# Optimization experiments

Hardware: AMD Instinct MI355X
Metric: run time of the kernel (lower is better)

## Reference

```python
import jax, jax.numpy as jnp
import numpy as np

X_DIM = 1024
HEADS = 16
EPS = 1e-5  # torch LayerNorm default


def setup_inputs() -> dict:
    key = jax.random.key(0)
    ks = jax.random.split(key, 4)
    B, N = 4, 1024
    x = jax.random.normal(ks[0], (B, N, X_DIM), jnp.float32)
    # torch nn.Linear weights are [out_features, in_features]; y = x @ W.T
    Wq = jax.random.normal(ks[1], (X_DIM, X_DIM), jnp.float32) * 0.02
    Wkv = jax.random.normal(ks[2], (2 * X_DIM, X_DIM), jnp.float32) * 0.02  # k_dim = x_dim + v_dim
    Wt = jax.random.normal(ks[3], (HEADS, HEADS), jnp.float32) * 0.25  # talk_h head-mixing
    ln_g = jnp.ones((HEADS,), jnp.float32)
    ln_b = jnp.zeros((HEADS,), jnp.float32)
    return {"x": x, "Wq": Wq, "Wkv": Wkv, "Wt": Wt, "ln_g": ln_g, "ln_b": ln_b}


def reference(x, Wq, Wkv, Wt, ln_g, ln_b):
    B, N, D = x.shape
    H = HEADS
    dh = D // H  # v head dim (= x head dim here since v_dim == x_dim)
    # projections
    q = (x @ Wq.T).reshape(B, N, H, dh).transpose(0, 2, 1, 3)  # b h i d
    kv = x @ Wkv.T  # [B, N, 2D]
    k = kv[..., :D].reshape(B, N, H, dh).transpose(0, 2, 1, 3)  # b h j d
    v = kv[..., D:].reshape(B, N, H, dh).transpose(0, 2, 1, 3)  # b h j d
    # scaled dot-product scores (scale uses x_dim, not head dim — faithful to source)
    dots = jnp.einsum('bhid,bhjd->bhij', q, k) * (D ** -0.5)
    w = jax.nn.softmax(dots, axis=-1)  # [B, H, N, N]
    # talk_h: ChSwap (transpose dims 1 and -1) -> Linear(heads) -> LayerNorm(heads) -> ChSwap
    wt = w.transpose(0, 3, 2, 1)  # b j i h
    wt = wt @ Wt.T
    mu = wt.mean(-1, keepdims=True)
    var = wt.var(-1, keepdims=True)
    wt = (wt - mu) / jnp.sqrt(var + EPS) * ln_g + ln_b
    w = wt.transpose(0, 3, 2, 1)  # back to b h i j
    # soft attention output
    attn = jnp.einsum('bhij,bhjd->bhid', w, v)
    # hard selection: argmax over keys, gather value rows
    idx = jnp.argmax(w, axis=-1)  # [B, H, N]
    hard = jnp.take_along_axis(v, jnp.broadcast_to(idx[..., None], idx.shape + (dh,)), axis=2)
    # straight-through: forward = hard, gradient flows through attn
    rtn = attn - jax.lax.stop_gradient(attn - hard)
    return rtn.transpose(0, 2, 1, 3).reshape(B, N, H * dh)
```

## Files before the change

### kernel.cpp

```cpp
#include <hip/hip_runtime.h>


#define FMA4(cc, av, bv) \
  cc.x = fmaf(av, bv.x, cc.x); cc.y = fmaf(av, bv.y, cc.y); \
  cc.z = fmaf(av, bv.z, cc.z); cc.w = fmaf(av, bv.w, cc.w);

__global__ __launch_bounds__(256) void qkv_gemm(
    const float* __restrict__ X, const float* __restrict__ Wq,
    const float* __restrict__ Wkv, float* __restrict__ qT,
    float* __restrict__ kT, float* __restrict__ V)
{
  __shared__ __align__(16) float As[16 * 132];
  __shared__ __align__(16) float Bs[16 * 132];
  __shared__ __align__(16) float tb[128 * 32];

  const int t  = threadIdx.x;
  const int bn = blockIdx.x;
  const int bm = blockIdx.y;
  const int m0 = bm * 128, n0 = bn * 128;
  const int ty = t >> 4, tx = t & 15;

  const float* Wbase = (n0 < 1024) ? Wq : Wkv;
  const int nw0 = (n0 < 1024) ? n0 : (n0 - 1024);

  float4 c2[8][2];
#pragma unroll
  for (int a = 0; a < 8; a++) {
    c2[a][0] = make_float4(0.f, 0.f, 0.f, 0.f);
    c2[a][1] = make_float4(0.f, 0.f, 0.f, 0.f);
  }

  const int lr = t >> 1;
  const int lh = t & 1;

  const float4* As4 = (const float4*)As;
  const float4* Bs4 = (const float4*)Bs;

  for (int kb = 0; kb < 64; kb++) {
    const int k0 = kb * 16;
    __syncthreads();
#pragma unroll
    for (int s = 0; s < 2; s++) {
      const int kk = lh * 8 + s * 4;
      float4 av = *(const float4*)&X[(size_t)(m0 + lr) * 1024 + k0 + kk];
      float4 bv = *(const float4*)&Wbase[(size_t)(nw0 + lr) * 1024 + k0 + kk];
      As[(kk + 0) * 132 + lr] = av.x;
      As[(kk + 1) * 132 + lr] = av.y;
      As[(kk + 2) * 132 + lr] = av.z;
      As[(kk + 3) * 132 + lr] = av.w;
      Bs[(kk + 0) * 132 + lr] = bv.x;
      Bs[(kk + 1) * 132 + lr] = bv.y;
      Bs[(kk + 2) * 132 + lr] = bv.z;
      Bs[(kk + 3) * 132 + lr] = bv.w;
    }
    __syncthreads();
#pragma unroll
    for (int kk = 0; kk < 16; kk++) {
      float4 a0 = As4[kk * 33 + ty * 2];
      float4 a1 = As4[kk * 33 + ty * 2 + 1];
      float4 b0 = Bs4[kk * 33 + tx];
      float4 b1 = Bs4[kk * 33 + 16 + tx];
      FMA4(c2[0][0], a0.x, b0); FMA4(c2[0][1], a0.x, b1);
      FMA4(c2[1][0], a0.y, b0); FMA4(c2[1][1], a0.y, b1);
      FMA4(c2[2][0], a0.z, b0); FMA4(c2[2][1], a0.z, b1);
      FMA4(c2[3][0], a0.w, b0); FMA4(c2[3][1], a0.w, b1);
      FMA4(c2[4][0], a1.x, b0); FMA4(c2[4][1], a1.x, b1);
      FMA4(c2[5][0], a1.y, b0); FMA4(c2[5][1], a1.y, b1);
      FMA4(c2[6][0], a1.z, b0); FMA4(c2[6][1], a1.z, b1);
      FMA4(c2[7][0], a1.w, b0); FMA4(c2[7][1], a1.w, b1);
    }
  }

  if (n0 >= 2048) {
    const int nv0 = n0 - 2048;
#pragma unroll
    for (int a = 0; a < 8; a++) {
      *(float4*)&V[(size_t)(m0 + ty * 8 + a) * 1024 + nv0 + tx * 4]      = c2[a][0];
      *(float4*)&V[(size_t)(m0 + ty * 8 + a) * 1024 + nv0 + 64 + tx * 4] = c2[a][1];
    }
    return;
  }

  float* T = (n0 < 1024) ? qT : kT;
  const int nt0 = (n0 < 1024) ? n0 : (n0 - 1024);
  const int bB = m0 >> 10;
  const int i0 = m0 & 1023;
#pragma unroll
  for (int r = 0; r < 4; r++) {
    __syncthreads();
    if ((tx >> 3) == (r & 1)) {
      const int c0 = (tx & 7) * 4;
#pragma unroll
      for (int a = 0; a < 8; a++) {
        const int m = ty * 8 + a;
        float4 val = c2[a][r >> 1];
        tb[m * 32 + ((c0 + 0 + m) & 31)] = val.x;
        tb[m * 32 + ((c0 + 1 + m) & 31)] = val.y;
        tb[m * 32 + ((c0 + 2 + m) & 31)] = val.z;
        tb[m * 32 + ((c0 + 3 + m) & 31)] = val.w;
      }
    }
    __syncthreads();
    const int nl = t >> 3, mq = t & 7;
    float* Trow = T + (size_t)(bB * 1024 + nt0 + (r >> 1) * 64 + (r & 1) * 32 + nl) * 1024 + i0;
#pragma unroll
    for (int l = 0; l < 4; l++) {
      const int mb = (l * 8 + mq) * 4;
      float4 o;
      o.x = tb[(mb + 0) * 32 + ((nl + mb + 0) & 31)];
      o.y = tb[(mb + 1) * 32 + ((nl + mb + 1) & 31)];
      o.z = tb[(mb + 2) * 32 + ((nl + mb + 2) & 31)];
      o.w = tb[(mb + 3) * 32 + ((nl + mb + 3) & 31)];
      *(float4*)(Trow + mb) = o;
    }
  }
}

__global__ __launch_bounds__(256) void attn_stats_v5(
    const float* __restrict__ qT, const float* __restrict__ kT,
    float* __restrict__ Mm, float* __restrict__ Ml)
{
  const int t  = threadIdx.x;
  const int bx = blockIdx.x;
  const int b  = bx >> 8;
  const int it = (bx >> 3) & 31;
  const int js = bx & 7;
  const int wv = t >> 6;
  const int l  = t & 63;
  const int ih = l >> 5;
  const int jg = l & 31;
  const int i0w = __builtin_amdgcn_readfirstlane(it * 32 + wv * 8);
  const int iq = i0w + ih * 4;
  const int jq = js * 128 + jg * 4;

  const float scale = 0.03125f;

  for (int h = 0; h < 16; h++) {
    const size_t base = (size_t)(b * 1024 + h * 64) * 1024;
    float4 acc[4];
#pragma unroll
    for (int ii = 0; ii < 4; ii++) acc[ii] = make_float4(0.f, 0.f, 0.f, 0.f);

#pragma unroll 4
    for (int d = 0; d < 64; d++) {
      const float4 qv = *(const float4*)(qT + base + (size_t)d * 1024 + iq);
      const float4 kv = *(const float4*)(kT + base + (size_t)d * 1024 + jq);
      FMA4(acc[0], qv.x, kv);
      FMA4(acc[1], qv.y, kv);
      FMA4(acc[2], qv.z, kv);
      FMA4(acc[3], qv.w, kv);
    }

#pragma unroll
    for (int ii = 0; ii < 4; ii++) {
      const float s0 = acc[ii].x * scale;
      const float s1 = acc[ii].y * scale;
      const float s2 = acc[ii].z * scale;
      const float s3 = acc[ii].w * scale;
      float mx = fmaxf(fmaxf(s0, s1), fmaxf(s2, s3));
      mx = fmaxf(mx, __shfl_xor(mx, 1));
      mx = fmaxf(mx, __shfl_xor(mx, 2));
      mx = fmaxf(mx, __shfl_xor(mx, 4));
      mx = fmaxf(mx, __shfl_xor(mx, 8));
      mx = fmaxf(mx, __shfl_xor(mx, 16));
      float ss = __expf(s0 - mx) + __expf(s1 - mx) +
                 __expf(s2 - mx) + __expf(s3 - mx);
      ss += __shfl_xor(ss, 1);
      ss += __shfl_xor(ss, 2);
      ss += __shfl_xor(ss, 4);
      ss += __shfl_xor(ss, 8);
      ss += __shfl_xor(ss, 16);
      if (jg == ii) {
        const int idx = (((b * 16 + h) * 1024 + iq + ii) << 3) + js;
        Mm[idx] = mx;
        Ml[idx] = ss;
      }
    }
  }
}

__global__ __launch_bounds__(256) void attn_stats_v6(
    const float* __restrict__ qT, const float* __restrict__ kT,
    float* __restrict__ Mm, float* __restrict__ Ml, float* __restrict__ Sp)
{
  const int t  = threadIdx.x;
  const int bx = blockIdx.x;
  const int b  = bx >> 8;
  const int it = (bx >> 3) & 31;
  const int js = bx & 7;
  const int wv = t >> 6;
  const int l  = t & 63;
  const int ih = l >> 5;
  const int jg = l & 31;
  const int i0w = __builtin_amdgcn_readfirstlane(it * 32 + wv * 8);
  const int iq = i0w + ih * 4;
  const int jq = js * 128 + jg * 4;

  const float scale = 0.03125f;

  for (int h = 0; h < 16; h++) {
    const size_t base = (size_t)(b * 1024 + h * 64) * 1024;
    float4 acc[4];
#pragma unroll
    for (int ii = 0; ii < 4; ii++) acc[ii] = make_float4(0.f, 0.f, 0.f, 0.f);

#pragma unroll 4
    for (int d = 0; d < 64; d++) {
      const float4 qv = *(const float4*)(qT + base + (size_t)d * 1024 + iq);
      const float4 kv = *(const float4*)(kT + base + (size_t)d * 1024 + jq);
      FMA4(acc[0], qv.x, kv);
      FMA4(acc[1], qv.y, kv);
      FMA4(acc[2], qv.z, kv);
      FMA4(acc[3], qv.w, kv);
    }

#pragma unroll
    for (int ii = 0; ii < 4; ii++) {
      const float s0 = acc[ii].x * scale;
      const float s1 = acc[ii].y * scale;
      const float s2 = acc[ii].z * scale;
      const float s3 = acc[ii].w * scale;
      float mx = fmaxf(fmaxf(s0, s1), fmaxf(s2, s3));
      mx = fmaxf(mx, __shfl_xor(mx, 1));
      mx = fmaxf(mx, __shfl_xor(mx, 2));
      mx = fmaxf(mx, __shfl_xor(mx, 4));
      mx = fmaxf(mx, __shfl_xor(mx, 8));
      mx = fmaxf(mx, __shfl_xor(mx, 16));
      const float e0 = __expf(s0 - mx);
      const float e1 = __expf(s1 - mx);
      const float e2 = __expf(s2 - mx);
      const float e3 = __expf(s3 - mx);
      *(float4*)&Sp[((size_t)((b * 16 + h) * 1024) + iq + ii) * 1024 + jq] =
          make_float4(e0, e1, e2, e3);
      float ss = e0 + e1 + e2 + e3;
      ss += __shfl_xor(ss, 1);
      ss += __shfl_xor(ss, 2);
      ss += __shfl_xor(ss, 4);
      ss += __shfl_xor(ss, 8);
      ss += __shfl_xor(ss, 16);
      if (jg == ii) {
        const int idx = (((b * 16 + h) * 1024 + iq + ii) << 3) + js;
        Mm[idx] = mx;
        Ml[idx] = ss;
      }
    }
  }
}

__device__ inline unsigned long long mkkey(float v, int j) {
  unsigned u = __float_as_uint(v);
  u = (u & 0x80000000u) ? ~u : (u | 0x80000000u);
  return ((unsigned long long)u << 32) | (unsigned)(1023 - j);
}

__global__ __launch_bounds__(256) void attn_select_v5(
    const float* __restrict__ qT, const float* __restrict__ kT,
    const float* __restrict__ Mm, const float* __restrict__ Ml,
    const float* __restrict__ Wt, const float* __restrict__ ln_g,
    const float* __restrict__ ln_b, unsigned long long* __restrict__ HiKey)
{
  __shared__ __align__(16) float smem[64 * 271 + 512];
  float* ptile = smem;
  float* mred  = smem + 64 * 271;
  float* rred  = mred + 256;

  const int t  = threadIdx.x;
  const int bx = blockIdx.x;
  const int b  = bx >> 10;
  const int it = (bx >> 4) & 63;
  const int js = bx & 15;
  const int i0 = it << 4;
  const int j0 = js << 6;

  const float scale = 0.03125f;

  {
    const int base = (((b * 16 + (t >> 4)) * 1024 + i0 + (t & 15)) << 3);
    const float4 ma = *(const float4*)&Mm[base];
    const float4 mb = *(const float4*)&Mm[base + 4];
    const float4 la = *(const float4*)&Ml[base];
    const float4 lb = *(const float4*)&Ml[base + 4];
    float M = fmaxf(fmaxf(fmaxf(ma.x, ma.y), fmaxf(ma.z, ma.w)),
                    fmaxf(fmaxf(mb.x, mb.y), fmaxf(mb.z, mb.w)));
    float L = la.x * __expf(ma.x - M) + la.y * __expf(ma.y - M) +
              la.z * __expf(ma.z - M) + la.w * __expf(ma.w - M) +
              lb.x * __expf(mb.x - M) + lb.y * __expf(mb.y - M) +
              lb.z * __expf(mb.z - M) + lb.w * __expf(mb.w - M);
    mred[t] = M;
    rred[t] = 1.0f / L;
  }
  __syncthreads();

  const int wv = t >> 6;
  const int l  = t & 63;
  const int jq = l & 15;
  const int ig = l >> 4;
  const int iq = i0 + ig * 4;
  const int jcol = j0 + jq * 4;

#pragma unroll
  for (int hl = 0; hl < 4; hl++) {
    const int h = wv * 4 + hl;
    const size_t base = (size_t)(b * 1024 + h * 64) * 1024;
    float4 acc[4];
#pragma unroll
    for (int ii = 0; ii < 4; ii++) acc[ii] = make_float4(0.f, 0.f, 0.f, 0.f);

#pragma unroll 4
    for (int d = 0; d < 64; d++) {
      const float4 qv = *(const float4*)(qT + base + (size_t)d * 1024 + iq);
      const float4 kv = *(const float4*)(kT + base + (size_t)d * 1024 + jcol);
      FMA4(acc[0], qv.x, kv);
      FMA4(acc[1], qv.y, kv);
      FMA4(acc[2], qv.z, kv);
      FMA4(acc[3], qv.w, kv);
    }

    const int hrot = (h + jq) & 15;
#pragma unroll
    for (int ii = 0; ii < 4; ii++) {
      const int iL = ig * 4 + ii;
      const float m = mred[h * 16 + iL];
      const float r = rred[h * 16 + iL];
      const float a4[4] = {acc[ii].x, acc[ii].y, acc[ii].z, acc[ii].w};
#pragma unroll
      for (int jj = 0; jj < 4; jj++) {
        const int j = jq * 4 + jj;
        const float p = __expf(a4[jj] * scale - m) * r;
        ptile[j * 271 + iL * 17 + hrot] = p;
      }
    }
  }
  __syncthreads();

  const int i2 = t >> 4;
  const int g  = (t >> 2) & 3;
  const int hq = t & 3;

  float wtr[4][16], gr[4], br[4];
#pragma unroll
  for (int a = 0; a < 4; a++) {
#pragma unroll
    for (int h2 = 0; h2 < 16; h2++) wtr[a][h2] = Wt[(hq * 4 + a) * 16 + h2];
    gr[a] = ln_g[hq * 4 + a];
    br[a] = ln_b[hq * 4 + a];
  }
  float bv[4]; int bix[4];
#pragma unroll
  for (int a = 0; a < 4; a++) { bv[a] = -1e30f; bix[a] = 0; }

#pragma unroll
  for (int jj = 0; jj < 16; jj++) {
    const int j = g * 16 + jj;
    const int jr = j >> 2;
    float pv[16];
#pragma unroll
    for (int h2 = 0; h2 < 16; h2++)
      pv[h2] = ptile[j * 271 + i2 * 17 + ((h2 + jr) & 15)];
    float mix[4];
#pragma unroll
    for (int a = 0; a < 4; a++) {
      float s0 = 0.f;
#pragma unroll
      for (int h2 = 0; h2 < 16; h2++) s0 = fmaf(pv[h2], wtr[a][h2], s0);
      mix[a] = s0;
    }
    float s1 = mix[0] + mix[1] + mix[2] + mix[3];
    s1 += __shfl_xor(s1, 1);
    s1 += __shfl_xor(s1, 2);
    const float mu = s1 * 0.0625f;
    float s2 = 0.f;
#pragma unroll
    for (int a = 0; a < 4; a++) { const float dd = mix[a] - mu; s2 = fmaf(dd, dd, s2); }
    s2 += __shfl_xor(s2, 1);
    s2 += __shfl_xor(s2, 2);
    const float rstd = rsqrtf(s2 * 0.0625f + 1e-5f);
    const int jg2 = j0 + j;
#pragma unroll
    for (int a = 0; a < 4; a++) {
      const float nv = (mix[a] - mu) * rstd * gr[a] + br[a];
      if (nv > bv[a]) { bv[a] = nv; bix[a] = jg2; }
    }
  }

#pragma unroll
  for (int a = 0; a < 4; a++) {
    float v = bv[a]; int ix = bix[a];
    {
      const float ov = __shfl_xor(v, 4);
      const int oi = __shfl_xor(ix, 4);
      if (ov > v || (ov == v && oi < ix)) { v = ov; ix = oi; }
    }
    {
      const float ov = __shfl_xor(v, 8);
      const int oi = __shfl_xor(ix, 8);
      if (ov > v || (ov == v && oi < ix)) { v = ov; ix = oi; }
    }
    bv[a] = v; bix[a] = ix;
  }

  if (g == 0) {
#pragma unroll
    for (int a = 0; a < 4; a++) {
      const int cell = (b * 16 + hq * 4 + a) * 1024 + i0 + i2;
      atomicMax(&HiKey[cell], mkkey(bv[a], bix[a]));
    }
  }
}

__global__ __launch_bounds__(256) void attn_select_v11(
    const float* __restrict__ Sp,
    const float* __restrict__ Mm, const float* __restrict__ Ml,
    const float* __restrict__ Wt, const float* __restrict__ ln_g,
    const float* __restrict__ ln_b, unsigned long long* __restrict__ HiKey)
{
  __shared__ __align__(16) float smem[64 * 271 + 256];
  float* ptile = smem;
  float* fred  = smem + 64 * 271;

  const int t  = threadIdx.x;
  const int bx = blockIdx.x;
  const int b  = bx >> 10;
  const int it = (bx >> 4) & 63;
  const int js = bx & 15;
  const int i0 = it << 4;
  const int j0 = js << 6;

  {
    const int base = (((b * 16 + (t >> 4)) * 1024 + i0 + (t & 15)) << 3);
    const float4 ma = *(const float4*)&Mm[base];
    const float4 mb = *(const float4*)&Mm[base + 4];
    const float4 la = *(const float4*)&Ml[base];
    const float4 lb = *(const float4*)&Ml[base + 4];
    float M = fmaxf(fmaxf(fmaxf(ma.x, ma.y), fmaxf(ma.z, ma.w)),
                    fmaxf(fmaxf(mb.x, mb.y), fmaxf(mb.z, mb.w)));
    float L = la.x * __expf(ma.x - M) + la.y * __expf(ma.y - M) +
              la.z * __expf(ma.z - M) + la.w * __expf(ma.w - M) +
              lb.x * __expf(mb.x - M) + lb.y * __expf(mb.y - M) +
              lb.z * __expf(mb.z - M) + lb.w * __expf(mb.w - M);
    const int si = js >> 1;
    const float4 mv = (si & 4) ? mb : ma;
    const int s2 = si & 3;
    const float msl = (s2 == 0) ? mv.x : (s2 == 1) ? mv.y
                    : (s2 == 2) ? mv.z : mv.w;
    fred[t] = __expf(msl - M) / L;
  }
  __syncthreads();

#pragma unroll
  for (int rr = 0; rr < 8; rr++) {
    const int rowid = rr * 32 + (t >> 3);
    const int h  = rowid >> 4;
    const int iL = rowid & 15;
    const int jseg = (t & 7) * 8;
    const float f = fred[rowid];
    const float* src = Sp + ((size_t)(b * 16 + h) * 1024 + i0 + iL) * 1024
                          + j0 + jseg;
    const float4 e0 = *(const float4*)src;
    const float4 e1 = *(const float4*)(src + 4);
    const float pv8[8] = {e0.x * f, e0.y * f, e0.z * f, e0.w * f,
                          e1.x * f, e1.y * f, e1.z * f, e1.w * f};
#pragma unroll
    for (int k = 0; k < 8; k++) {
      const int j = jseg + k;
      ptile[j * 271 + iL * 17 + ((h + (j >> 2)) & 15)] = pv8[k];
    }
  }
  __syncthreads();

  const int i2 = t >> 4;
  const int g  = (t >> 2) & 3;
  const int hq = t & 3;

  float wtr[4][16], gr[4], br[4];
#pragma unroll
  for (int a = 0; a < 4; a++) {
#pragma unroll
    for (int h2 = 0; h2 < 16; h2++) wtr[a][h2] = Wt[(hq * 4 + a) * 16 + h2];
    gr[a] = ln_g[hq * 4 + a];
    br[a] = ln_b[hq * 4 + a];
  }
  float bv[4]; int bix[4];
#pragma unroll
  for (int a = 0; a < 4; a++) { bv[a] = -1e30f; bix[a] = 0; }

#pragma unroll
  for (int jj = 0; jj < 16; jj++) {
    const int j = g * 16 + jj;
    const int jr = j >> 2;
    float pv[16];
#pragma unroll
    for (int h2 = 0; h2 < 16; h2++)
      pv[h2] = ptile[j * 271 + i2 * 17 + ((h2 + jr) & 15)];
    float mix[4];
#pragma unroll
    for (int a = 0; a < 4; a++) {
      float s0 = 0.f;
#pragma unroll
      for (int h2 = 0; h2 < 16; h2++) s0 = fmaf(pv[h2], wtr[a][h2], s0);
      mix[a] = s0;
    }
    float s1 = mix[0] + mix[1] + mix[2] + mix[3];
    s1 += __shfl_xor(s1, 1);
    s1 += __shfl_xor(s1, 2);
    const float mu = s1 * 0.0625f;
    float s2 = 0.f;
#pragma unroll
    for (int a = 0; a < 4; a++) { const float dd = mix[a] - mu; s2 = fmaf(dd, dd, s2); }
    s2 += __shfl_xor(s2, 1);
    s2 += __shfl_xor(s2, 2);
    const float rstd = rsqrtf(s2 * 0.0625f + 1e-5f);
    const int jg2 = j0 + j;
#pragma unroll
    for (int a = 0; a < 4; a++) {
      const float nv = (mix[a] - mu) * rstd * gr[a] + br[a];
      if (nv > bv[a]) { bv[a] = nv; bix[a] = jg2; }
    }
  }

#pragma unroll
  for (int a = 0; a < 4; a++) {
    float v = bv[a]; int ix = bix[a];
    {
      const float ov = __shfl_xor(v, 4);
      const int oi = __shfl_xor(ix, 4);
      if (ov > v || (ov == v && oi < ix)) { v = ov; ix = oi; }
    }
    {
      const float ov = __shfl_xor(v, 8);
      const int oi = __shfl_xor(ix, 8);
      if (ov > v || (ov == v && oi < ix)) { v = ov; ix = oi; }
    }
    bv[a] = v; bix[a] = ix;
  }

  if (g == 0) {
#pragma unroll
    for (int a = 0; a < 4; a++) {
      const int cell = (b * 16 + hq * 4 + a) * 1024 + i0 + i2;
      atomicMax(&HiKey[cell], mkkey(bv[a], bix[a]));
    }
  }
}

__global__ __launch_bounds__(256) void gather_v4(
    const unsigned long long* __restrict__ HiKey, const float* __restrict__ V,
    float* __restrict__ out)
{
  const int t  = threadIdx.x;
  const int bx = blockIdx.x;
  const int b  = bx >> 6;
  const int it = bx & 63;
  const int i2 = t >> 4;
  const int h  = t & 15;

  const unsigned long long key = HiKey[(b * 16 + h) * 1024 + it * 16 + i2];
  const int j = 1023 - (int)(unsigned)(key & 0xFFFFFFFFull);

  const float* vs = V + (size_t)(b * 1024 + j) * 1024 + h * 64;
  float* dst = out + (size_t)(b * 1024 + it * 16 + i2) * 1024 + h * 64;
#pragma unroll
  for (int w = 0; w < 16; w++)
    *(float4*)(dst + w * 4) = *(const float4*)(vs + w * 4);
}

extern "C" void kernel_launch(void* const* d_in, const int* in_sizes, int n_in,
                              void* d_out, int out_size, void* d_ws, size_t ws_size,
                              hipStream_t stream) {
  const float* x   = (const float*)d_in[0];
  const float* Wq  = (const float*)d_in[1];
  const float* Wkv = (const float*)d_in[2];
  const float* Wt  = (const float*)d_in[3];
  const float* lng = (const float*)d_in[4];
  const float* lnb = (const float*)d_in[5];
  float* out = (float*)d_out;
  float* ws  = (float*)d_ws;
  float* qT = ws;
  float* kT = ws + (size_t)4 * 1024 * 1024;
  float* V  = ws + (size_t)8 * 1024 * 1024;
  float* Mm = ws + (size_t)12 * 1024 * 1024;
  float* Ml = Mm + 524288;
  unsigned long long* HiKey =
      (unsigned long long*)(ws + (size_t)13 * 1024 * 1024);
  float* Sp = ws + (size_t)14 * 1024 * 1024;

  const size_t NEED = (size_t)78 * 1024 * 1024 * 4;
  const bool big_ws = (ws_size >= NEED);

  hipLaunchKernelGGL(qkv_gemm, dim3(24, 32), dim3(256), 0, stream,
                     x, Wq, Wkv, qT, kT, V);
  hipMemsetAsync(HiKey, 0, (size_t)65536 * 8, stream);
  if (big_ws) {
    hipLaunchKernelGGL(attn_stats_v6, dim3(1024), dim3(256), 0, stream,
                       qT, kT, Mm, Ml, Sp);
    hipLaunchKernelGGL(attn_select_v11, dim3(4096), dim3(256), 0, stream,
                       Sp, Mm, Ml, Wt, lng, lnb, HiKey);
  } else {
    hipLaunchKernelGGL(attn_stats_v5, dim3(1024), dim3(256), 0, stream,
                       qT, kT, Mm, Ml);
    hipLaunchKernelGGL(attn_select_v5, dim3(4096), dim3(256), 0, stream,
                       qT, kT, Mm, Ml, Wt, lng, lnb, HiKey);
  }
  hipLaunchKernelGGL(gather_v4, dim3(256), dim3(256), 0, stream,
                     HiKey, V, out);
}
```

Baseline: 978.9 us.

## Split the score-materialising attention path per batch to shrink the workspace

The stats and select kernels on the large-workspace path now run once per batch in a host loop. This shrinks the exp-score buffer Sp from all four batches to a single batch, cutting the workspace requirement so the path is used more often, and the smaller buffer may stay resident in the last-level cache between write and read. The cost is more kernel launches and a stats grid of only 256 blocks per launch, which lowers occupancy. Separately, the fallback select kernel now computes two heads per loop iteration for more instruction-level parallelism.

```diff
diff --git a/kernel.cpp b/kernel.cpp
--- a/kernel.cpp
+++ b/kernel.cpp
@@ -179,14 +179,14 @@
   }
 }
 
-__global__ __launch_bounds__(256) void attn_stats_v6(
+__global__ __launch_bounds__(256) void attn_stats_v6b(
     const float* __restrict__ qT, const float* __restrict__ kT,
-    float* __restrict__ Mm, float* __restrict__ Ml, float* __restrict__ Sp)
+    float* __restrict__ Mm, float* __restrict__ Ml,
+    float* __restrict__ Sp, int b)
 {
   const int t  = threadIdx.x;
   const int bx = blockIdx.x;
-  const int b  = bx >> 8;
-  const int it = (bx >> 3) & 31;
+  const int it = bx >> 3;
   const int js = bx & 7;
   const int wv = t >> 6;
   const int l  = t & 63;
@@ -230,7 +230,7 @@
       const float e1 = __expf(s1 - mx);
       const float e2 = __expf(s2 - mx);
       const float e3 = __expf(s3 - mx);
-      *(float4*)&Sp[((size_t)((b * 16 + h) * 1024) + iq + ii) * 1024 + jq] =
+      *(float4*)&Sp[((size_t)(h * 1024) + iq + ii) * 1024 + jq] =
           make_float4(e0, e1, e2, e3);
       float ss = e0 + e1 + e2 + e3;
       ss += __shfl_xor(ss, 1);
@@ -253,7 +253,7 @@
   return ((unsigned long long)u << 32) | (unsigned)(1023 - j);
 }
 
-__global__ __launch_bounds__(256) void attn_select_v5(
+__global__ __launch_bounds__(256) void attn_select_v12(
     const float* __restrict__ qT, const float* __restrict__ kT,
     const float* __restrict__ Mm, const float* __restrict__ Ml,
     const float* __restrict__ Wt, const float* __restrict__ ln_g,
@@ -299,35 +299,50 @@
   const int jcol = j0 + jq * 4;
 
 #pragma unroll
-  for (int hl = 0; hl < 4; hl++) {
-    const int h = wv * 4 + hl;
-    const size_t base = (size_t)(b * 1024 + h * 64) * 1024;
-    float4 acc[4];
-#pragma unroll
-    for (int ii = 0; ii < 4; ii++) acc[ii] = make_float4(0.f, 0.f, 0.f, 0.f);
-
-#pragma unroll 4
+  for (int r = 0; r < 2; r++) {
+    const int hA = wv * 4 + r * 2;
+    const size_t baseA = (size_t)(b * 1024 + hA * 64) * 1024;
+    const size_t baseB = baseA + (size_t)64 * 1024;
+    float4 accA[4], accB[4];
+#pragma unroll
+    for (int ii = 0; ii < 4; ii++) {
+      accA[ii] = make_float4(0.f, 0.f, 0.f, 0.f);
+      accB[ii] = make_float4(0.f, 0.f, 0.f, 0.f);
+    }
+
+#pragma unroll 2
     for (int d = 0; d < 64; d++) {
-      const float4 qv = *(const float4*)(qT + base + (size_t)d * 1024 + iq);
-      const float4 kv = *(const float4*)(kT + base + (size_t)d * 1024 + jcol);
-      FMA4(acc[0], qv.x, kv);
-      FMA4(acc[1], qv.y, kv);
-      FMA4(acc[2], qv.z, kv);
-      FMA4(acc[3], qv.w, kv);
-    }
-
-    const int hrot = (h + jq) & 15;
-#pragma unroll
-    for (int ii = 0; ii < 4; ii++) {
-      const int iL = ig * 4 + ii;
-      const float m = mred[h * 16 + iL];
-      const float r = rred[h * 16 + iL];
-      const float a4[4] = {acc[ii].x, acc[ii].y, acc[ii].z, acc[ii].w};
-#pragma unroll
-      for (int jj = 0; jj < 4; jj++) {
-        const int j = jq * 4 + jj;
-        const float p = __expf(a4[jj] * scale - m) * r;
-        ptile[j * 271 + iL * 17 + hrot] = p;
+      const float4 qA = *(const float4*)(qT + baseA + (size_t)d * 1024 + iq);
+      const float4 kA = *(const float4*)(kT + baseA + (size_t)d * 1024 + jcol);
+      const float4 qB = *(const float4*)(qT + baseB + (size_t)d * 1024 + iq);
+      const float4 kB = *(const float4*)(kT + baseB + (size_t)d * 1024 + jcol);
+      FMA4(accA[0], qA.x, kA);
+      FMA4(accA[1], qA.y, kA);
+      FMA4(accA[2], qA.z, kA);
+      FMA4(accA[3], qA.w, kA);
+      FMA4(accB[0], qB.x, kB);
+      FMA4(accB[1], qB.y, kB);
+      FMA4(accB[2], qB.z, kB);
+      FMA4(accB[3], qB.w, kB);
+    }
+
+#pragma unroll
+    for (int hs = 0; hs < 2; hs++) {
+      const int h = hA + hs;
+      const float4* acc = hs ? accB : accA;
+      const int hrot = (h + jq) & 15;
+#pragma unroll
+      for (int ii = 0; ii < 4; ii++) {
+        const int iL = ig * 4 + ii;
+        const float m = mred[h * 16 + iL];
+        const float rr = rred[h * 16 + iL];
+        const float a4[4] = {acc[ii].x, acc[ii].y, acc[ii].z, acc[ii].w};
+#pragma unroll
+        for (int jj = 0; jj < 4; jj++) {
+          const int j = jq * 4 + jj;
+          const float p = __expf(a4[jj] * scale - m) * rr;
+          ptile[j * 271 + iL * 17 + hrot] = p;
+        }
       }
     }
   }
@@ -408,11 +423,12 @@
   }
 }
 
-__global__ __launch_bounds__(256) void attn_select_v11(
+__global__ __launch_bounds__(256) void attn_select_v11b(
     const float* __restrict__ Sp,
     const float* __restrict__ Mm, const float* __restrict__ Ml,
     const float* __restrict__ Wt, const float* __restrict__ ln_g,
-    const float* __restrict__ ln_b, unsigned long long* __restrict__ HiKey)
+    const float* __restrict__ ln_b, unsigned long long* __restrict__ HiKey,
+    int b)
 {
   __shared__ __align__(16) float smem[64 * 271 + 256];
   float* ptile = smem;
@@ -420,8 +436,7 @@
 
   const int t  = threadIdx.x;
   const int bx = blockIdx.x;
-  const int b  = bx >> 10;
-  const int it = (bx >> 4) & 63;
+  const int it = bx >> 4;
   const int js = bx & 15;
   const int i0 = it << 4;
   const int j0 = js << 6;
@@ -454,8 +469,7 @@
     const int iL = rowid & 15;
     const int jseg = (t & 7) * 8;
     const float f = fred[rowid];
-    const float* src = Sp + ((size_t)(b * 16 + h) * 1024 + i0 + iL) * 1024
-                          + j0 + jseg;
+    const float* src = Sp + ((size_t)(h * 1024) + i0 + iL) * 1024 + j0 + jseg;
     const float4 e0 = *(const float4*)src;
     const float4 e1 = *(const float4*)(src + 4);
     const float pv8[8] = {e0.x * f, e0.y * f, e0.z * f, e0.w * f,
@@ -584,21 +598,23 @@
       (unsigned long long*)(ws + (size_t)13 * 1024 * 1024);
   float* Sp = ws + (size_t)14 * 1024 * 1024;
 
-  const size_t NEED = (size_t)78 * 1024 * 1024 * 4;
+  const size_t NEED = (size_t)30 * 1024 * 1024 * 4;
   const bool big_ws = (ws_size >= NEED);
 
   hipLaunchKernelGGL(qkv_gemm, dim3(24, 32), dim3(256), 0, stream,
                      x, Wq, Wkv, qT, kT, V);
   hipMemsetAsync(HiKey, 0, (size_t)65536 * 8, stream);
   if (big_ws) {
-    hipLaunchKernelGGL(attn_stats_v6, dim3(1024), dim3(256), 0, stream,
-                       qT, kT, Mm, Ml, Sp);
-    hipLaunchKernelGGL(attn_select_v11, dim3(4096), dim3(256), 0, stream,
-                       Sp, Mm, Ml, Wt, lng, lnb, HiKey);
+    for (int b = 0; b < 4; b++) {
+      hipLaunchKernelGGL(attn_stats_v6b, dim3(256), dim3(256), 0, stream,
+                         qT, kT, Mm, Ml, Sp, b);
+      hipLaunchKernelGGL(attn_select_v11b, dim3(1024), dim3(256), 0, stream,
+                         Sp, Mm, Ml, Wt, lng, lnb, HiKey, b);
+    }
   } else {
     hipLaunchKernelGGL(attn_stats_v5, dim3(1024), dim3(256), 0, stream,
                        qT, kT, Mm, Ml);
-    hipLaunchKernelGGL(attn_select_v5, dim3(4096), dim3(256), 0, stream,
+    hipLaunchKernelGGL(attn_select_v12, dim3(4096), dim3(256), 0, stream,
                        qT, kT, Mm, Ml, Wt, lng, lnb, HiKey);
   }
   hipLaunchKernelGGL(gather_v4, dim3(256), dim3(256), 0, stream,
```

After: 1.679 ms. 71.5% more time.
